# Kernel tuning notes

Hardware: AMD Instinct MI355X
Metric: run time of the kernel (lower is better)

Reference implementation:

```python
import jax, jax.numpy as jnp
import numpy as np

QUERY_DIM = 1024
KEY_DIM = 1024
NUM_HEADS = 16
HEAD_DIM = QUERY_DIM // NUM_HEADS


def setup_inputs() -> dict:
    key = jax.random.key(0)
    ks = jax.random.split(key, 11)
    B, Sq, Sk = 2, 2048, 2048
    s = 0.02
    return {
        "q": jax.random.normal(ks[0], (B, Sq, QUERY_DIM), jnp.float32),
        "k": jax.random.normal(ks[1], (B, Sk, KEY_DIM), jnp.float32),
        "v": jax.random.normal(ks[2], (B, Sk, KEY_DIM), jnp.float32),
        "Wq": jax.random.normal(ks[3], (QUERY_DIM, QUERY_DIM), jnp.float32) * s,
        "bq": jnp.zeros((QUERY_DIM,), jnp.float32),
        "Wk": jax.random.normal(ks[4], (KEY_DIM, QUERY_DIM), jnp.float32) * s,
        "bk": jnp.zeros((QUERY_DIM,), jnp.float32),
        "Wv": jax.random.normal(ks[5], (KEY_DIM, QUERY_DIM), jnp.float32) * s,
        "bv": jnp.zeros((QUERY_DIM,), jnp.float32),
        "Wo": jax.random.normal(ks[6], (QUERY_DIM, QUERY_DIM), jnp.float32) * s,
        "bo": jnp.zeros((QUERY_DIM,), jnp.float32),
    }


def reference(q, k, v, Wq, bq, Wk, bk, Wv, bv, Wo, bo):
    B, Sq, _ = q.shape
    Sk = k.shape[1]
    scale = HEAD_DIM ** -0.5
    # projections -> [B, H, S, Dh]
    qh = (q @ Wq + bq).reshape(B, Sq, NUM_HEADS, HEAD_DIM).transpose(0, 2, 1, 3)
    kh = (k @ Wk + bk).reshape(B, Sk, NUM_HEADS, HEAD_DIM).transpose(0, 2, 1, 3)
    vh = (v @ Wv + bv).reshape(B, Sk, NUM_HEADS, HEAD_DIM).transpose(0, 2, 1, 3)
    scores = jnp.einsum("bhqd,bhkd->bhqk", qh, kh) * scale
    attn = jax.nn.softmax(scores, axis=-1)
    out = jnp.einsum("bhqk,bhkd->bhqd", attn, vh)
    out = out.transpose(0, 2, 1, 3).reshape(B, Sq, QUERY_DIM)
    return out @ Wo + bo  # dropout is identity at inference
```

## Files before the change

kernel.cpp:

```cpp
#include <hip/hip_runtime.h>
#include <hip/hip_fp16.h>
#include <cstddef>


#define B_   2
#define S_   2048
#define D_   1024
#define H_   16
#define DH_  64

typedef _Float16 half8 __attribute__((ext_vector_type(8)));
typedef _Float16 half4 __attribute__((ext_vector_type(4)));
typedef float floatx4 __attribute__((ext_vector_type(4)));

#define MFMA32(a, b, c) __builtin_amdgcn_mfma_f32_16x16x32_f16((a), (b), (c), 0, 0, 0)
#define MFMA16(a, b, c) __builtin_amdgcn_mfma_f32_16x16x16f16((a), (b), (c), 0, 0, 0)

__global__ __launch_bounds__(256) void cvt3(
    const float* __restrict__ q, const float* __restrict__ k,
    const float* __restrict__ v,
    __half* __restrict__ qf, __half* __restrict__ kf, __half* __restrict__ vf)
{
    const float* srcs[3] = {q, k, v};
    __half* dsts[3] = {qf, kf, vf};
    const int z = blockIdx.y;
    const int i = blockIdx.x * 256 + threadIdx.x;
    const float4* s = (const float4*)srcs[z];
    const float4 a = s[2 * i], b = s[2 * i + 1];
    half8 h;
    h[0] = (_Float16)a.x; h[1] = (_Float16)a.y; h[2] = (_Float16)a.z; h[3] = (_Float16)a.w;
    h[4] = (_Float16)b.x; h[5] = (_Float16)b.y; h[6] = (_Float16)b.z; h[7] = (_Float16)b.w;
    *(half8*)&dsts[z][(size_t)i * 8] = h;
}

__global__ __launch_bounds__(256) void wtrans4(
    const float* __restrict__ Wq, const float* __restrict__ Wk,
    const float* __restrict__ Wv, const float* __restrict__ Wo,
    __half* __restrict__ Wtq, __half* __restrict__ Wtk,
    __half* __restrict__ Wtv, __half* __restrict__ Wto)
{
    __shared__ __align__(16) __half T[64][72];
    const float* Ws[4] = {Wq, Wk, Wv, Wo};
    __half* Wts[4] = {Wtq, Wtk, Wtv, Wto};
    const float* W = Ws[blockIdx.z];
    __half* Wt = Wts[blockIdx.z];
    const int tid = threadIdx.x;
    const int n0 = blockIdx.x * 64, k0 = blockIdx.y * 64;
    #pragma unroll
    for (int p = 0; p < 4; ++p) {
        const int c = tid + p * 256;
        const int kr = c >> 4, nc = (c & 15) * 4;
        const float4 a = *(const float4*)&W[(size_t)(k0 + kr) * D_ + n0 + nc];
        T[nc + 0][kr] = __float2half(a.x);
        T[nc + 1][kr] = __float2half(a.y);
        T[nc + 2][kr] = __float2half(a.z);
        T[nc + 3][kr] = __float2half(a.w);
    }
    __syncthreads();
    #pragma unroll
    for (int p = 0; p < 2; ++p) {
        const int c = tid + p * 256;
        const int nr = c >> 3, kc = (c & 7) * 8;
        *(half8*)&Wt[(size_t)(n0 + nr) * D_ + k0 + kc] = *(const half8*)&T[nr][kc];
    }
}

__device__ __forceinline__ void gemm_core(
    const __half* __restrict__ A, const __half* __restrict__ Bt,
    const float* __restrict__ bias, void* __restrict__ dst,
    const int mode, const float oscale)
{
    __shared__ __align__(16) char gsm[36864];
    __half (*As)[72] = (__half(*)[72])gsm;
    __half (*Bs)[72] = (__half(*)[72])(gsm + 18432);

    const int tid = threadIdx.x;
    const int m0 = blockIdx.y * 128, n0 = blockIdx.x * 128;
    const int lane = tid & 63, wv = tid >> 6;
    const int quad = lane >> 4, lr = lane & 15;
    const int wm0 = (wv >> 1) * 64, wn0 = (wv & 1) * 64;

    floatx4 acc[4][4];
    #pragma unroll
    for (int i = 0; i < 4; ++i)
        #pragma unroll
        for (int j = 0; j < 4; ++j)
            acc[i][j] = (floatx4){0.f, 0.f, 0.f, 0.f};

    half8 pa[4], pb[4];
    #pragma unroll
    for (int p = 0; p < 4; ++p) {
        const int c = tid + p * 256;
        const int row = c >> 3, seg = (c & 7) * 8;
        pa[p] = *(const half8*)&A [(size_t)(m0 + row) * D_ + seg];
        pb[p] = *(const half8*)&Bt[(size_t)(n0 + row) * D_ + seg];
    }

    for (int k0 = 0; k0 < D_; k0 += 64) {
        __syncthreads();
        #pragma unroll
        for (int p = 0; p < 4; ++p) {
            const int c = tid + p * 256;
            const int row = c >> 3, seg = (c & 7) * 8;
            *(half8*)&As[row][seg] = pa[p];
            *(half8*)&Bs[row][seg] = pb[p];
        }
        if (k0 + 64 < D_) {
            #pragma unroll
            for (int p = 0; p < 4; ++p) {
                const int c = tid + p * 256;
                const int row = c >> 3, seg = (c & 7) * 8;
                pa[p] = *(const half8*)&A [(size_t)(m0 + row) * D_ + k0 + 64 + seg];
                pb[p] = *(const half8*)&Bt[(size_t)(n0 + row) * D_ + k0 + 64 + seg];
            }
        }
        __syncthreads();
        #pragma unroll
        for (int ks = 0; ks < 2; ++ks) {
            const int ko = quad * 8 + ks * 32;
            half8 af[4], bf[4];
            #pragma unroll
            for (int i = 0; i < 4; ++i) af[i] = *(const half8*)&As[wm0 + i * 16 + lr][ko];
            #pragma unroll
            for (int j = 0; j < 4; ++j) bf[j] = *(const half8*)&Bs[wn0 + j * 16 + lr][ko];
            #pragma unroll
            for (int i = 0; i < 4; ++i)
                #pragma unroll
                for (int j = 0; j < 4; ++j)
                    acc[i][j] = MFMA32(af[i], bf[j], acc[i][j]);
        }
    }

    if (mode == 1) {
        float* out = (float*)dst;
        #pragma unroll
        for (int i = 0; i < 4; ++i) {
            #pragma unroll
            for (int j = 0; j < 4; ++j) {
                const int col = n0 + wn0 + j * 16 + lr;
                const float bval = bias[col];
                #pragma unroll
                for (int r = 0; r < 4; ++r) {
                    const int m = m0 + wm0 + i * 16 + quad * 4 + r;
                    out[(size_t)m * D_ + col] = acc[i][j][r] + bval;
                }
            }
        }
        return;
    }

    __syncthreads();
    __half (*Ct)[136] = (__half(*)[136])gsm;
    #pragma unroll
    for (int i = 0; i < 4; ++i) {
        #pragma unroll
        for (int j = 0; j < 4; ++j) {
            const int nl = wn0 + j * 16 + lr;
            const float bval = bias[n0 + nl];
            #pragma unroll
            for (int r = 0; r < 4; ++r) {
                const int ml = wm0 + i * 16 + quad * 4 + r;
                const _Float16 hv = (_Float16)((acc[i][j][r] + bval) * oscale);
                if (mode == 0) Ct[ml][nl] = hv;
                else           Ct[nl][ml] = hv;
            }
        }
    }
    __syncthreads();
    __half* oh = (__half*)dst;
    #pragma unroll
    for (int p = 0; p < 8; ++p) {
        const int row = (tid >> 4) + p * 16;
        const int cs  = (tid & 15) * 8;
        const half8 vls = *(const half8*)&Ct[row][cs];
        if (mode == 0) {
            const int m = m0 + row, col = n0 + cs;
            const int b = m >> 11, s = m & (S_ - 1);
            const int h = col >> 6, d = col & 63;
            *(half8*)&oh[(((size_t)(b * H_ + h) * S_ + s) << 6) + d] = vls;
        } else {
            const int col = n0 + row, m = m0 + cs;
            const int b = m >> 11, s = m & (S_ - 1);
            const int h = col >> 6, d = col & 63;
            *(half8*)&oh[((size_t)(b * H_ + h) * DH_ + d) * S_ + s] = vls;
        }
    }
}

__global__ __launch_bounds__(256) void gemm_proj(
    const __half* __restrict__ qf, const __half* __restrict__ kf,
    const __half* __restrict__ vf,
    const __half* __restrict__ Wtq, const __half* __restrict__ Wtk,
    const __half* __restrict__ Wtv,
    const float* __restrict__ bq, const float* __restrict__ bk,
    const float* __restrict__ bv,
    __half* __restrict__ qhf, __half* __restrict__ khf, __half* __restrict__ vht)
{
    const __half* As[3] = {qf, kf, vf};
    const __half* Bts[3] = {Wtq, Wtk, Wtv};
    const float* bs[3] = {bq, bk, bv};
    __half* ds[3] = {qhf, khf, vht};
    const int z = blockIdx.z;
    gemm_core(As[z], Bts[z], bs[z], ds[z], z == 2 ? 2 : 0, z == 0 ? 0.125f : 1.0f);
}

__global__ __launch_bounds__(256) void gemm_final(
    const __half* __restrict__ attf, const __half* __restrict__ Wto,
    const float* __restrict__ bo, float* __restrict__ out)
{
    gemm_core(attf, Wto, bo, out, 1, 1.0f);
}

__global__ __launch_bounds__(256) void attn_f16(
    const __half* __restrict__ qhf, const __half* __restrict__ khf,
    const __half* __restrict__ vht, __half* __restrict__ attf)
{
    __shared__ __align__(16) char smem[31232];
    __half (*Qs)[72] = (__half(*)[72])smem;
    __half (*Ks)[72] = (__half(*)[72])(smem + 9216);
    __half (*Vs)[72] = (__half(*)[72])(smem + 18432);

    const int tid = threadIdx.x;
    const int lane = tid & 63, wv = tid >> 6;
    const int quad = lane >> 4, lr = lane & 15;
    const int bh = blockIdx.y;
    const int q0 = blockIdx.x * 64;
    const size_t hbase = (size_t)bh * S_ * DH_;

    #pragma unroll
    for (int p = 0; p < 2; ++p) {
        const int c = tid + p * 256;
        const int row = c >> 3, seg = (c & 7) * 8;
        *(half8*)&Qs[row][seg] = *(const half8*)&qhf[hbase + (size_t)(q0 + row) * DH_ + seg];
    }
    __syncthreads();
    half8 qB[4][2];
    #pragma unroll
    for (int qs = 0; qs < 4; ++qs)
        #pragma unroll
        for (int ks = 0; ks < 2; ++ks)
            qB[qs][ks] = *(const half8*)&Qs[qs * 16 + lr][quad * 8 + ks * 32];

    float lp[4] = {0.f, 0.f, 0.f, 0.f};
    floatx4 O[4][4];
    #pragma unroll
    for (int i = 0; i < 4; ++i)
        #pragma unroll
        for (int j = 0; j < 4; ++j)
            O[i][j] = (floatx4){0.f, 0.f, 0.f, 0.f};

    half8 pk[2], pv[2];
    #pragma unroll
    for (int p = 0; p < 2; ++p) {
        const int c = tid + p * 256;
        const int row = c >> 3, seg = (c & 7) * 8;
        pk[p] = *(const half8*)&khf[hbase + (size_t)row * DH_ + seg];
        pv[p] = *(const half8*)&vht[hbase + (size_t)row * S_ + seg];
    }

    for (int kt = 0; kt < S_; kt += 64) {
        __syncthreads();
        #pragma unroll
        for (int p = 0; p < 2; ++p) {
            const int c = tid + p * 256;
            const int row = c >> 3, seg = (c & 7) * 8;
            *(half8*)&Ks[row][seg] = pk[p];
            *(half8*)&Vs[row][seg] = pv[p];
        }
        if (kt + 64 < S_) {
            #pragma unroll
            for (int p = 0; p < 2; ++p) {
                const int c = tid + p * 256;
                const int row = c >> 3, seg = (c & 7) * 8;
                pk[p] = *(const half8*)&khf[hbase + (size_t)(kt + 64 + row) * DH_ + seg];
                pv[p] = *(const half8*)&vht[hbase + (size_t)row * S_ + kt + 64 + seg];
            }
        }
        __syncthreads();

        floatx4 s4[4];
        #pragma unroll
        for (int qs = 0; qs < 4; ++qs) s4[qs] = (floatx4){0.f, 0.f, 0.f, 0.f};
        #pragma unroll
        for (int ks = 0; ks < 2; ++ks) {
            const half8 aK = *(const half8*)&Ks[wv * 16 + lr][quad * 8 + ks * 32];
            #pragma unroll
            for (int qs = 0; qs < 4; ++qs)
                s4[qs] = MFMA32(aK, qB[qs][ks], s4[qs]);
        }

        half4 pB[4];
        #pragma unroll
        for (int qs = 0; qs < 4; ++qs) {
            #pragma unroll
            for (int r = 0; r < 4; ++r) {
                const float p = __expf(s4[qs][r]);
                lp[qs] += p;
                pB[qs][r] = (_Float16)p;
            }
        }

        #pragma unroll
        for (int ds = 0; ds < 4; ++ds) {
            const half4 aV = *(const half4*)&Vs[ds * 16 + lr][wv * 16 + quad * 4];
            #pragma unroll
            for (int qs = 0; qs < 4; ++qs)
                O[ds][qs] = MFMA16(aV, pB[qs], O[ds][qs]);
        }
    }

    __syncthreads();
    float* L    = (float*)(smem + 17408);
    float* invL = (float*)(smem + 21504);
    float (*R)[68] = (float(*)[68])smem;
    __half (*F)[72] = (__half(*)[72])(smem + 22016);

    #pragma unroll
    for (int qs = 0; qs < 4; ++qs)
        L[(wv * 4 + quad) * 64 + qs * 16 + lr] = lp[qs];
    __syncthreads();
    if (tid < 64) {
        float s = 0.f;
        #pragma unroll
        for (int i = 0; i < 16; ++i) s += L[i * 64 + tid];
        invL[tid] = 1.0f / s;
    }
    __syncthreads();

    const int qc = tid & 63, dg = tid >> 6;
    const float il = invL[qc];

    #pragma unroll
    for (int ds = 0; ds < 4; ++ds) {
        __syncthreads();
        #pragma unroll
        for (int qs = 0; qs < 4; ++qs)
            #pragma unroll
            for (int r = 0; r < 4; ++r)
                R[wv * 16 + quad * 4 + r][qs * 16 + lr] = O[ds][qs][r];
        __syncthreads();
        half4 hv;
        #pragma unroll
        for (int rr = 0; rr < 4; ++rr) {
            const int row = dg * 4 + rr;
            const float v = R[row][qc] + R[16 + row][qc] + R[32 + row][qc] + R[48 + row][qc];
            hv[rr] = (_Float16)(v * il);
        }
        *(half4*)&F[qc][ds * 16 + dg * 4] = hv;
    }
    __syncthreads();

    const int b = bh >> 4, h = bh & 15;
    const int qrow = tid >> 2, dseg = (tid & 3) * 16;
    __half* dstp = &attf[(((size_t)(b * S_ + q0 + qrow)) << 10) + h * DH_ + dseg];
    *(half8*)&dstp[0] = *(const half8*)&F[qrow][dseg];
    *(half8*)&dstp[8] = *(const half8*)&F[qrow][dseg + 8];
}

extern "C" void kernel_launch(void* const* d_in, const int* in_sizes, int n_in,
                              void* d_out, int out_size, void* d_ws, size_t ws_size,
                              hipStream_t stream) {
    const float* q  = (const float*)d_in[0];
    const float* k  = (const float*)d_in[1];
    const float* v  = (const float*)d_in[2];
    const float* Wq = (const float*)d_in[3];
    const float* bq = (const float*)d_in[4];
    const float* Wk = (const float*)d_in[5];
    const float* bk = (const float*)d_in[6];
    const float* Wv = (const float*)d_in[7];
    const float* bv = (const float*)d_in[8];
    const float* Wo = (const float*)d_in[9];
    const float* bo = (const float*)d_in[10];
    float* out = (float*)d_out;

    __half* ws = (__half*)d_ws;
    const size_t NE = (size_t)B_ * S_ * D_;
    __half* qf   = ws;
    __half* kf   = ws + NE;
    __half* vf   = ws + 2 * NE;
    __half* qhf  = ws + 3 * NE;
    __half* khf  = ws + 4 * NE;
    __half* vht  = ws + 5 * NE;
    __half* attf = ws + 6 * NE;
    __half* Wtq  = ws + 7 * NE;
    __half* Wtk  = Wtq + (size_t)D_ * D_;
    __half* Wtv  = Wtk + (size_t)D_ * D_;
    __half* Wto  = Wtv + (size_t)D_ * D_;

    const dim3 blk(256);
    cvt3<<<dim3((unsigned)(NE / 8 / 256), 3), blk, 0, stream>>>(q, k, v, qf, kf, vf);
    wtrans4<<<dim3(16, 16, 4), blk, 0, stream>>>(Wq, Wk, Wv, Wo, Wtq, Wtk, Wtv, Wto);

    gemm_proj<<<dim3(D_ / 128, (B_ * S_) / 128, 3), blk, 0, stream>>>(
        qf, kf, vf, Wtq, Wtk, Wtv, bq, bk, bv, qhf, khf, vht);

    attn_f16<<<dim3(S_ / 64, B_ * H_), blk, 0, stream>>>(qhf, khf, vht, attf);

    gemm_final<<<dim3(D_ / 128, (B_ * S_) / 128), blk, 0, stream>>>(attf, Wto, bo, out);
}
```

Before: 233.5 us.

## Load GEMM tiles directly into LDS and fold log2e into Q scaling

```diff
diff --git a/kernel.cpp b/kernel.cpp
--- a/kernel.cpp
+++ b/kernel.cpp
@@ -15,6 +15,12 @@
 
 #define MFMA32(a, b, c) __builtin_amdgcn_mfma_f32_16x16x32_f16((a), (b), (c), 0, 0, 0)
 #define MFMA16(a, b, c) __builtin_amdgcn_mfma_f32_16x16x16f16((a), (b), (c), 0, 0, 0)
+
+__device__ __forceinline__ void gload16(const void* g, void* l) {
+    __builtin_amdgcn_global_load_lds(
+        (const __attribute__((address_space(1))) unsigned int*)g,
+        (__attribute__((address_space(3))) unsigned int*)l, 16, 0, 0);
+}
 
 __global__ __launch_bounds__(256) void cvt3(
     const float* __restrict__ q, const float* __restrict__ k,
@@ -70,9 +76,9 @@
     const float* __restrict__ bias, void* __restrict__ dst,
     const int mode, const float oscale)
 {
-    __shared__ __align__(16) char gsm[36864];
-    __half (*As)[72] = (__half(*)[72])gsm;
-    __half (*Bs)[72] = (__half(*)[72])(gsm + 18432);
+    __shared__ __align__(16) char gsm[34816];
+    __half* As = (__half*)gsm;
+    __half* Bs = (__half*)(gsm + 16384);
 
     const int tid = threadIdx.x;
     const int m0 = blockIdx.y * 128, n0 = blockIdx.x * 128;
@@ -80,6 +86,10 @@
     const int quad = lane >> 4, lr = lane & 15;
     const int wm0 = (wv >> 1) * 64, wn0 = (wv & 1) * 64;
 
+    const int crow = tid >> 3;
+    const int cseg = (tid & 7) * 8;
+    const int wbase16 = (tid & 192) * 16;
+
     floatx4 acc[4][4];
     #pragma unroll
     for (int i = 0; i < 4; ++i)
@@ -87,48 +97,30 @@
         for (int j = 0; j < 4; ++j)
             acc[i][j] = (floatx4){0.f, 0.f, 0.f, 0.f};
 
-    half8 pa[4], pb[4];
-    #pragma unroll
-    for (int p = 0; p < 4; ++p) {
-        const int c = tid + p * 256;
-        const int row = c >> 3, seg = (c & 7) * 8;
-        pa[p] = *(const half8*)&A [(size_t)(m0 + row) * D_ + seg];
-        pb[p] = *(const half8*)&Bt[(size_t)(n0 + row) * D_ + seg];
-    }
-
     for (int k0 = 0; k0 < D_; k0 += 64) {
-        __syncthreads();
         #pragma unroll
         for (int p = 0; p < 4; ++p) {
-            const int c = tid + p * 256;
-            const int row = c >> 3, seg = (c & 7) * 8;
-            *(half8*)&As[row][seg] = pa[p];
-            *(half8*)&Bs[row][seg] = pb[p];
-        }
-        if (k0 + 64 < D_) {
-            #pragma unroll
-            for (int p = 0; p < 4; ++p) {
-                const int c = tid + p * 256;
-                const int row = c >> 3, seg = (c & 7) * 8;
-                pa[p] = *(const half8*)&A [(size_t)(m0 + row) * D_ + k0 + 64 + seg];
-                pb[p] = *(const half8*)&Bt[(size_t)(n0 + row) * D_ + k0 + 64 + seg];
-            }
-        }
-        __syncthreads();
+            const int row = crow + p * 32;
+            gload16(&A [(size_t)(m0 + row) * D_ + k0 + cseg], gsm + p * 4096 + wbase16);
+            gload16(&Bt[(size_t)(n0 + row) * D_ + k0 + cseg], gsm + 16384 + p * 4096 + wbase16);
+        }
+        __syncthreads();
+
         #pragma unroll
         for (int ks = 0; ks < 2; ++ks) {
             const int ko = quad * 8 + ks * 32;
             half8 af[4], bf[4];
             #pragma unroll
-            for (int i = 0; i < 4; ++i) af[i] = *(const half8*)&As[wm0 + i * 16 + lr][ko];
-            #pragma unroll
-            for (int j = 0; j < 4; ++j) bf[j] = *(const half8*)&Bs[wn0 + j * 16 + lr][ko];
+            for (int i = 0; i < 4; ++i) af[i] = *(const half8*)&As[(wm0 + i * 16 + lr) * 64 + ko];
+            #pragma unroll
+            for (int j = 0; j < 4; ++j) bf[j] = *(const half8*)&Bs[(wn0 + j * 16 + lr) * 64 + ko];
             #pragma unroll
             for (int i = 0; i < 4; ++i)
                 #pragma unroll
                 for (int j = 0; j < 4; ++j)
                     acc[i][j] = MFMA32(af[i], bf[j], acc[i][j]);
         }
+        __syncthreads();
     }
 
     if (mode == 1) {
@@ -149,7 +141,6 @@
         return;
     }
 
-    __syncthreads();
     __half (*Ct)[136] = (__half(*)[136])gsm;
     #pragma unroll
     for (int i = 0; i < 4; ++i) {
@@ -201,7 +192,8 @@
     const float* bs[3] = {bq, bk, bv};
     __half* ds[3] = {qhf, khf, vht};
     const int z = blockIdx.z;
-    gemm_core(As[z], Bts[z], bs[z], ds[z], z == 2 ? 2 : 0, z == 0 ? 0.125f : 1.0f);
+    gemm_core(As[z], Bts[z], bs[z], ds[z], z == 2 ? 2 : 0,
+              z == 0 ? 0.1803368801111244f : 1.0f);
 }
 
 __global__ __launch_bounds__(256) void gemm_final(
@@ -294,7 +286,7 @@
         for (int qs = 0; qs < 4; ++qs) {
             #pragma unroll
             for (int r = 0; r < 4; ++r) {
-                const float p = __expf(s4[qs][r]);
+                const float p = exp2f(s4[qs][r]);
                 lp[qs] += p;
                 pB[qs][r] = (_Float16)p;
             }
```

Result: slower. 267.1 us (+14.4%).
